# Performance work log

Measured on AMD Instinct MI355X. Metric: run time of the kernel, lower is better.

Reference implementation:

```python
import jax, jax.numpy as jnp
import numpy as np

N0, N1, N2, N3 = 8192, 32768, 65536, 65536
CUM = (N0, N0 + N1, N0 + N1 + N2, N0 + N1 + N2 + N3)  # nodes through hop k
NTOT = CUM[3]
EH = (131072, 262144, 262144)                          # edges per hop (per edge type)
ECUM = (EH[0], EH[0] + EH[1], EH[0] + EH[1] + EH[2])
ETOT = ECUM[2]
C, H, T = 64, 256, 3
HH = H // 2
B, L = 16, 512  # N0 == B * L: equal-length note sequences per graph
LN_EPS = 1e-5


def _ln(x, w, b):
    m = x.mean(-1, keepdims=True)
    v = x.var(-1, keepdims=True)
    return (x - m) / jnp.sqrt(v + LN_EPS) * w + b


def _seg_mean(msgs, dst, n):
    s = jax.ops.segment_sum(msgs, dst, num_segments=n)
    cnt = jax.ops.segment_sum(jnp.ones(dst.shape, msgs.dtype), dst, num_segments=n)
    return s / jnp.maximum(cnt, 1.0)[:, None]


def _l2(x):
    return x / jnp.maximum(jnp.linalg.norm(x, axis=-1, keepdims=True), 1e-12)


def _gru_dir(x, wih, whh, bih, bhh, reverse):
    # x: [B, Lt, Din]; torch gate order (r, z, n)
    gi = jnp.einsum('bld,gd->blg', x, wih) + bih
    gi = jnp.moveaxis(gi, 1, 0)  # [Lt, B, 3*HH]
    h0 = jnp.zeros((x.shape[0], HH), x.dtype)

    def step(h, g):
        gh = h @ whh.T + bhh
        ir, iz, in_ = jnp.split(g, 3, -1)
        hr, hz, hn = jnp.split(gh, 3, -1)
        r = jax.nn.sigmoid(ir + hr)
        z = jax.nn.sigmoid(iz + hz)
        n = jnp.tanh(in_ + r * hn)
        hnew = (1.0 - z) * n + z * h
        return hnew, hnew

    _, ys = jax.lax.scan(step, h0, gi, reverse=reverse)
    return jnp.moveaxis(ys, 0, 1)  # [B, Lt, HH]


def _bigru(x, wih, whh, bih, bhh):
    f = _gru_dir(x, wih[0], whh[0], bih[0], bhh[0], False)
    bwd = _gru_dir(x, wih[1], whh[1], bih[1], bhh[1], True)
    return jnp.concatenate([f, bwd], -1)


def _forward(x, edge_index, batch_size, sage0_proj_w, sage0_proj_b, sage0_lw, sage0_lb,
             sage0_rw, sage_lw, sage_lb, sage_rw, ln_w, ln_b,
             gru_wih0, gru_whh0, gru_bih0, gru_bhh0,
             gru_wih1, gru_whh1, gru_bih1, gru_bhh1,
             rnn_norm_w, rnn_norm_b, mlp1_w, mlp1_b, mlp_ln_w, mlp_ln_b,
             mlp2_w, mlp2_b, cat_w, cat_b):
    # ---- hybrid GRU branch on seed notes (equal lengths -> pad == reshape) ----
    xs = x[:batch_size].reshape(B, L, C)
    h = _bigru(xs, gru_wih0, gru_whh0, gru_bih0, gru_bhh0)
    h = _bigru(h, gru_wih1, gru_whh1, gru_bih1, gru_bhh1)  # inter-layer dropout: eval mode
    h = _ln(h, rnn_norm_w, rnn_norm_b)
    h = _ln(jax.nn.relu(h @ mlp1_w + mlp1_b), mlp_ln_w, mlp_ln_b) @ mlp2_w + mlp2_b
    x_rnn = h.reshape(batch_size, H)

    # ---- GNN layer 0: SAGEConv(project=True, normalize=True), hetero mean over T types ----
    feat = x
    outs = []
    for t in range(T):
        src, dst = edge_index[t, 0], edge_index[t, 1]
        xp = jax.nn.relu(feat @ sage0_proj_w[t] + sage0_proj_b[t])
        agg = _seg_mean(xp[src], dst, NTOT)
        outs.append(_l2(agg @ sage0_lw[t] + sage0_lb[t] + feat @ sage0_rw[t]))
    feat = sum(outs) / T
    feat = _ln(jax.nn.relu(feat), ln_w[0], ln_b[0])  # dropout: eval mode (identity)

    # ---- layers 1..2 with trim_to_layer: drop last sampled hop each layer ----
    n_layer = (CUM[2], CUM[1])
    e_layer = (ECUM[1], ECUM[0])
    for i in range(2):
        n, e = n_layer[i], e_layer[i]
        feat = feat[:n]
        outs = []
        for t in range(T):
            src, dst = edge_index[t, 0, :e], edge_index[t, 1, :e]
            agg = _seg_mean(feat[src], dst, n)
            outs.append(agg @ sage_lw[i, t] + sage_lb[i, t] + feat @ sage_rw[i, t])
        feat = sum(outs) / T
        if i == 0:
            feat = _ln(jax.nn.relu(feat), ln_w[1], ln_b[1])
    x_gnn = feat[:batch_size]
    return jnp.concatenate([x_rnn, x_gnn], -1) @ cat_w + cat_b


def setup_inputs():
    key = jax.random.key(0)
    ks = iter(jax.random.split(key, 64))

    def nrm(shape, fan_in):
        return jax.random.normal(next(ks), shape, jnp.float32) / float(np.sqrt(fan_in))

    # hop-structured edges: hop k has src < CUM[k+1], dst < CUM[k]
    ei = []
    for t in range(T):
        rows, cols = [], []
        for k in range(3):
            rows.append(jax.random.randint(next(ks), (EH[k],), 0, CUM[k + 1]))
            cols.append(jax.random.randint(next(ks), (EH[k],), 0, CUM[k]))
        ei.append(jnp.stack([jnp.concatenate(rows), jnp.concatenate(cols)]))
    edge_index = jnp.stack(ei).astype(jnp.int32)

    return dict(
        x=jax.random.normal(next(ks), (NTOT, C), jnp.float32),
        edge_index=edge_index,
        batch=(jnp.arange(N0) // L).astype(jnp.int32),
        batch_size=N0,
        sage0_proj_w=nrm((T, C, C), C), sage0_proj_b=jnp.zeros((T, C), jnp.float32),
        sage0_lw=nrm((T, C, H), C), sage0_lb=jnp.zeros((T, H), jnp.float32),
        sage0_rw=nrm((T, C, H), C),
        sage_lw=nrm((2, T, H, H), H), sage_lb=jnp.zeros((2, T, H), jnp.float32),
        sage_rw=nrm((2, T, H, H), H),
        ln_w=jnp.ones((2, H), jnp.float32), ln_b=jnp.zeros((2, H), jnp.float32),
        gru_wih0=nrm((2, 3 * HH, C), C), gru_whh0=nrm((2, 3 * HH, HH), HH),
        gru_bih0=jnp.zeros((2, 3 * HH), jnp.float32), gru_bhh0=jnp.zeros((2, 3 * HH), jnp.float32),
        gru_wih1=nrm((2, 3 * HH, H), H), gru_whh1=nrm((2, 3 * HH, HH), HH),
        gru_bih1=jnp.zeros((2, 3 * HH), jnp.float32), gru_bhh1=jnp.zeros((2, 3 * HH), jnp.float32),
        rnn_norm_w=jnp.ones((H,), jnp.float32), rnn_norm_b=jnp.zeros((H,), jnp.float32),
        mlp1_w=nrm((H, H), H), mlp1_b=jnp.zeros((H,), jnp.float32),
        mlp_ln_w=jnp.ones((H,), jnp.float32), mlp_ln_b=jnp.zeros((H,), jnp.float32),
        mlp2_w=nrm((H, H), H), mlp2_b=jnp.zeros((H,), jnp.float32),
        cat_w=nrm((2 * H, H), 2 * H), cat_b=jnp.zeros((H,), jnp.float32),
    )


def reference(x, edge_index, batch, batch_size, sage0_proj_w, sage0_proj_b, sage0_lw,
              sage0_lb, sage0_rw, sage_lw, sage_lb, sage_rw, ln_w, ln_b,
              gru_wih0, gru_whh0, gru_bih0, gru_bhh0, gru_wih1, gru_whh1, gru_bih1,
              gru_bhh1, rnn_norm_w, rnn_norm_b, mlp1_w, mlp1_b, mlp_ln_w, mlp_ln_b,
              mlp2_w, mlp2_b, cat_w, cat_b):
    # batch encodes 16 equal-length (512) sequences; bincount/pad == reshape above
    return _forward(x, edge_index, batch_size, sage0_proj_w, sage0_proj_b, sage0_lw,
                    sage0_lb, sage0_rw, sage_lw, sage_lb, sage_rw, ln_w, ln_b,
                    gru_wih0, gru_whh0, gru_bih0, gru_bhh0, gru_wih1, gru_whh1,
                    gru_bih1, gru_bhh1, rnn_norm_w, rnn_norm_b, mlp1_w, mlp1_b,
                    mlp_ln_w, mlp_ln_b, mlp2_w, mlp2_b, cat_w, cat_b)
```

## Files before the change

kernel.cpp:

```cpp
#include <hip/hip_runtime.h>
#include <stdint.h>

typedef unsigned short u16;
typedef __attribute__((ext_vector_type(8))) short short8;
typedef __attribute__((ext_vector_type(4))) short short4v;
typedef __attribute__((ext_vector_type(4))) float float4v;

#define DEV static __device__ __forceinline__

DEV float bf2f(u16 u){ union { unsigned int i; float f; } c; c.i = ((unsigned int)u) << 16; return c.f; }
DEV u16 f2bf(float f){ union { float ff; unsigned int i; } c; c.ff = f;
  unsigned int x = c.i; return (u16)((x + 0x7fffu + ((x >> 16) & 1u)) >> 16); }

#define MFMA16(a,b,c) __builtin_amdgcn_mfma_f32_16x16x32_bf16((a),(b),(c),0,0,0)

#define ETOTC  655360
#define TSTRIDE 155648
#define NBINS   466944

struct SM {
  u16 As[64*72];
  u16 Bs[256*72];
  float redS[4][64];
  float redQ[4][64];
  float rowA[64], rowB[64];
};

__global__ void detect_dtype(const u16* __restrict__ xs, int* __restrict__ flag){
  __shared__ int sh[256];
  int t = threadIdx.x; int cnt = 0;
  for (int i = t; i < 4096; i += 256){
    u16 u = xs[i]; int e = (u >> 7) & 0xff;
    cnt += (u == 0 || (e >= 112 && e <= 143)) ? 1 : 0;
  }
  sh[t] = cnt; __syncthreads();
  for (int d = 128; d; d >>= 1){ if (t < d) sh[t] += sh[t+d]; __syncthreads(); }
  if (t == 0) flag[0] = (sh[0] >= 3686) ? 1 : 0;
}

DEV u16 scrub(u16 v){ int e = (v >> 7) & 0xff; return (e == 0xff) ? (u16)0 : v; }

__global__ void convert_x(const void* __restrict__ xin, const int* __restrict__ flag,
                          u16* __restrict__ out){
  int i = blockIdx.x*256 + threadIdx.x;
  u16 v[4];
  if (flag[0] == 1){
    short4v s = ((const short4v*)xin)[i];
#pragma unroll
    for (int j=0;j<4;j++) v[j] = scrub((u16)s[j]);
  } else {
    float4v f = ((const float4v*)xin)[i];
#pragma unroll
    for (int j=0;j<4;j++) v[j] = scrub(f2bf(f[j]));
  }
  short4v o; o[0]=(short)v[0]; o[1]=(short)v[1]; o[2]=(short)v[2]; o[3]=(short)v[3];
  ((short4v*)out)[i] = o;
}

struct WSrc { const void* p[28]; };
__device__ const int g_wcum[29] = {0,12288,12480,61632,62400,111552,504768,506304,899520,
  900032,900544,949696,1048000,1048768,1049536,1246144,1344448,1345216,1345984,1346240,
  1346496,1412032,1412288,1412544,1412800,1478336,1478592,1609664,1609920};

__global__ void convert_w(WSrc d, const int* __restrict__ flag, u16* __restrict__ out){
  int i = blockIdx.x*256 + threadIdx.x;
  if (i >= 1609920) return;
  int lo = 0, hi = 28;
  while (hi - lo > 1){ int m = (lo+hi) >> 1; if (i >= g_wcum[m]) lo = m; else hi = m; }
  int off = i - g_wcum[lo];
  u16 v = (flag[0] == 1) ? ((const u16*)d.p[lo])[off]
                         : f2bf(((const float*)d.p[lo])[off]);
  out[i] = scrub(v);
}

__global__ void packT(const u16* __restrict__ in, u16* __restrict__ out, int K, int N){
  int i = blockIdx.x*256 + threadIdx.x;
  if (i < K*N){ int n = i / K, k = i - n*K; out[i] = in[(size_t)k*N + n]; }
}

__global__ void pack_lr(const u16* __restrict__ lw, const u16* __restrict__ rw,
                        u16* __restrict__ out, int F){
  int K2 = 2*F; long total = 3L*256*K2;
  long i = (long)blockIdx.x*256 + threadIdx.x;
  if (i < total){
    int k = (int)(i % K2); int n = (int)((i / K2) & 255); int t = (int)(i / ((long)K2*256));
    out[i] = (k < F) ? lw[((size_t)t*F + k)*256 + n]
                     : rw[((size_t)t*F + (k-F))*256 + n];
  }
}

DEV void hist_body(int gb, const int* __restrict__ ei, int* __restrict__ cnt){
  int g = gb*256 + threadIdx.x;
  int t = g / ETOTC, e = g - t*ETOTC;
  int dst = ei[(size_t)t*2*ETOTC + ETOTC + e];
  int base = t*TSTRIDE;
  atomicAdd(&cnt[base + dst], 1);
  if (e < 393216) atomicAdd(&cnt[base + 106496 + dst], 1);
  if (e < 131072) atomicAdd(&cnt[base + 147456 + dst], 1);
}

DEV void perm_body(int gb, const int* __restrict__ ei, const int* __restrict__ off,
                   int* __restrict__ slot, int* __restrict__ srcs){
  int g = gb*256 + threadIdx.x;
  int t = g / ETOTC, e = g - t*ETOTC;
  int dst = ei[(size_t)t*2*ETOTC + ETOTC + e];
  int src = ei[(size_t)t*2*ETOTC + e];
  int base = t*TSTRIDE;
  { int b = base + dst; srcs[off[b] + atomicAdd(&slot[b], 1)] = src; }
  if (e < 393216){ int b = base + 106496 + dst;
    srcs[off[b] + atomicAdd(&slot[b], 1)] = src; }
  if (e < 131072){ int b = base + 147456 + dst;
    srcs[off[b] + atomicAdd(&slot[b], 1)] = src; }
}

__global__ void scan_blocks(const int* __restrict__ cnt, int* __restrict__ off,
                            int* __restrict__ bsum, int n){
  __shared__ int sh[256];
  int t = threadIdx.x;
  int base = blockIdx.x*2048 + t*8;
  int v[8]; int tot = 0;
#pragma unroll
  for (int j=0;j<8;j++){ v[j] = (base+j < n) ? cnt[base+j] : 0; tot += v[j]; }
  sh[t] = tot; __syncthreads();
  for (int d=1; d<256; d<<=1){
    int y = (t>=d) ? sh[t-d] : 0; __syncthreads();
    sh[t] += y; __syncthreads();
  }
  int run = sh[t] - tot;
#pragma unroll
  for (int j=0;j<8;j++){ if (base+j < n) off[base+j] = run; run += v[j]; }
  if (t == 255) bsum[blockIdx.x] = sh[255];
}

__global__ void scan_top(int* __restrict__ bsum, int G){
  __shared__ int sh[256];
  int t = threadIdx.x;
  int v = (t < G) ? bsum[t] : 0;
  sh[t] = v; __syncthreads();
  for (int d=1; d<256; d<<=1){
    int y = (t>=d) ? sh[t-d] : 0; __syncthreads();
    sh[t] += y; __syncthreads();
  }
  if (t < G) bsum[t] = sh[t] - v;
}

__global__ void scan_add(int* __restrict__ off, const int* __restrict__ bsum, int n){
  int add = bsum[blockIdx.x];
  int base = blockIdx.x*2048 + threadIdx.x*8;
#pragma unroll
  for (int j=0;j<8;j++) if (base+j < n) off[base+j] += add;
}

template<int F>
DEV void gather_body(int w, int lane,
    const int* __restrict__ off, const int* __restrict__ cnt, const int* __restrict__ srcs,
    const u16* __restrict__ feat, int ld, u16* __restrict__ out)
{
  int st = off[w], c = cnt[w];
  float sc = 1.f / (float)(c < 1 ? 1 : c);
  if (F == 64) {
    float a = 0.f, b = 0.f;
    int i = 0;
    for (; i + 4 <= c; i += 4){
      int s0 = srcs[st+i], s1 = srcs[st+i+1], s2 = srcs[st+i+2], s3 = srcs[st+i+3];
      u16 u0 = feat[(size_t)s0*ld + lane];
      u16 u1 = feat[(size_t)s1*ld + lane];
      u16 u2 = feat[(size_t)s2*ld + lane];
      u16 u3 = feat[(size_t)s3*ld + lane];
      a += bf2f(u0) + bf2f(u1);
      b += bf2f(u2) + bf2f(u3);
    }
    for (; i < c; ++i){ int s = srcs[st+i]; a += bf2f(feat[(size_t)s*ld + lane]); }
    out[(size_t)w*64 + lane] = f2bf((a + b)*sc);
  } else {
    float a0=0.f,a1=0.f,a2=0.f,a3=0.f;
    float b0=0.f,b1=0.f,b2=0.f,b3=0.f;
    int i = 0;
    for (; i + 4 <= c; i += 4){
      int s0 = srcs[st+i], s1 = srcs[st+i+1], s2 = srcs[st+i+2], s3 = srcs[st+i+3];
      short4v u0 = *(const short4v*)(feat + (size_t)s0*ld + lane*4);
      short4v u1 = *(const short4v*)(feat + (size_t)s1*ld + lane*4);
      short4v u2 = *(const short4v*)(feat + (size_t)s2*ld + lane*4);
      short4v u3 = *(const short4v*)(feat + (size_t)s3*ld + lane*4);
      a0 += bf2f((u16)u0[0]) + bf2f((u16)u1[0]);
      a1 += bf2f((u16)u0[1]) + bf2f((u16)u1[1]);
      a2 += bf2f((u16)u0[2]) + bf2f((u16)u1[2]);
      a3 += bf2f((u16)u0[3]) + bf2f((u16)u1[3]);
      b0 += bf2f((u16)u2[0]) + bf2f((u16)u3[0]);
      b1 += bf2f((u16)u2[1]) + bf2f((u16)u3[1]);
      b2 += bf2f((u16)u2[2]) + bf2f((u16)u3[2]);
      b3 += bf2f((u16)u2[3]) + bf2f((u16)u3[3]);
    }
    for (; i < c; ++i){
      int s = srcs[st+i];
      short4v u = *(const short4v*)(feat + (size_t)s*ld + lane*4);
      a0 += bf2f((u16)u[0]); a1 += bf2f((u16)u[1]);
      a2 += bf2f((u16)u[2]); a3 += bf2f((u16)u[3]);
    }
    u16* o = out + (size_t)w*256 + lane*4;
    o[0]=f2bf((a0+b0)*sc); o[1]=f2bf((a1+b1)*sc);
    o[2]=f2bf((a2+b2)*sc); o[3]=f2bf((a3+b3)*sc);
  }
}

DEV void ln_body(int r, int lane,
    const u16* __restrict__ in, u16* __restrict__ out,
    const u16* __restrict__ w, const u16* __restrict__ b)
{
  short4v u = *(const short4v*)(in + (size_t)r*256 + lane*4);
  float v[4];
#pragma unroll
  for (int i=0;i<4;i++) v[i] = bf2f((u16)u[i]);
  float s = v[0]+v[1]+v[2]+v[3];
  float q = v[0]*v[0]+v[1]*v[1]+v[2]*v[2]+v[3]*v[3];
#pragma unroll
  for (int d=1; d<64; d<<=1){ s += __shfl_xor(s, d); q += __shfl_xor(q, d); }
  float mu = s * (1.f/256.f);
  float var = fmaxf(q * (1.f/256.f) - mu*mu, 0.f);
  float rs = rsqrtf(var + 1e-5f);
  u16* o = out + (size_t)r*256 + lane*4;
#pragma unroll
  for (int i=0;i<4;i++){
    int col = lane*4 + i;
    o[i] = f2bf((v[i]-mu)*rs*bf2f(w[col]) + bf2f(b[col]));
  }
}

#define LGKM0_SB do{ asm volatile("s_waitcnt lgkmcnt(0)" ::: "memory"); \
                     __builtin_amdgcn_sched_barrier(0); \
                     __builtin_amdgcn_s_barrier(); \
                     __builtin_amdgcn_sched_barrier(0); }while(0)

#define GRU_STEP(S, C0, C1, C2) do{                                          \
    const int l_ = dir ? (511 - (S)) : (S);                                  \
    short8 afr_[4];                                                          \
    _Pragma("unroll")                                                        \
    for (int kt=0; kt<4; kt++) afr_[kt] = *(const short8*)(&hbf[kt*32 + lg*8]); \
    float4v acc_[4];                                                         \
    _Pragma("unroll")                                                        \
    for (int nt=0; nt<4; nt++) acc_[nt] = (float4v){0.f,0.f,0.f,0.f};        \
    _Pragma("unroll")                                                        \
    for (int kt=0; kt<4; kt++){                                              \
      _Pragma("unroll")                                                      \
      for (int nt=0; nt<4; nt++) acc_[nt] = MFMA16(afr_[kt], bfrag[nt][kt], acc_[nt]); } \
    if (lane < 16){                                                          \
      _Pragma("unroll")                                                      \
      for (int nt=0; nt<4; nt++) ghs[64*w + nt*16 + lane] = acc_[nt][0];     \
    }                                                                        \
    LGKM0_SB;                                                                \
    if (tid < 128){                                                          \
      float ghr = ghs[tid]       + bhr;                                      \
      float ghz = ghs[128 + tid] + bhz;                                      \
      float ghn = ghs[256 + tid] + bhn;                                      \
      float r_ = 1.f/(1.f + __expf(-((C0) + ghr)));                          \
      float z_ = 1.f/(1.f + __expf(-((C1) + ghz)));                          \
      float xn_ = (C2) + r_*ghn;                                             \
      float th_ = 1.f - 2.f/(__expf(2.f*xn_) + 1.f);                         \
      hreg = (1.f - z_)*th_ + z_*hreg;                                       \
      u16 hb_ = f2bf(hreg);                                                  \
      hbf[tid] = hb_;                                                        \
      hout[((size_t)(b*512 + l_))*256 + dir*128 + tid] = hb_;                \
      int sn_ = (S) + 2;                                                     \
      if (sn_ < 512){                                                        \
        int ln2_ = dir ? (511 - sn_) : sn_;                                  \
        const float* g_ = gbase + (size_t)ln2_*768;                          \
        (C0) = g_[0]; (C1) = g_[128]; (C2) = g_[256];                        \
      }                                                                      \
    }                                                                        \
    LGKM0_SB;                                                                \
  }while(0)

DEV void gru_body(const float* __restrict__ gi, const u16* __restrict__ whh,
                  const u16* __restrict__ bhh, u16* __restrict__ hout,
                  int bid, u16* hbf, float* ghs)
{
  const int b = bid >> 1, dir = bid & 1;
  const int tid = threadIdx.x;
  const int w = tid >> 6, lane = tid & 63;
  const int lr = lane & 15, lg = lane >> 4;

  short8 bfrag[4][4];
#pragma unroll
  for (int nt=0; nt<4; nt++)
#pragma unroll
    for (int kt=0; kt<4; kt++){
      int n = 64*w + nt*16 + lr;
      bfrag[nt][kt] = *(const short8*)(whh + ((size_t)(dir*384 + n))*128 + kt*32 + lg*8);
    }

  const float* gbase = gi + (size_t)b*512*768 + dir*384 + tid;
  float hreg = 0.f, bhr = 0.f, bhz = 0.f, bhn = 0.f;
  float a0=0.f,a1=0.f,a2=0.f, e0=0.f,e1=0.f,e2=0.f;
  if (tid < 128){
    bhr = bf2f(bhh[dir*384 + tid]);
    bhz = bf2f(bhh[dir*384 + 128 + tid]);
    bhn = bf2f(bhh[dir*384 + 256 + tid]);
    const float* g0 = gbase + (size_t)(dir ? 511 : 0)*768;
    a0 = g0[0]; a1 = g0[128]; a2 = g0[256];
    const float* g1 = gbase + (size_t)(dir ? 510 : 1)*768;
    e0 = g1[0]; e1 = g1[128]; e2 = g1[256];
  }
  if (tid < 64) ((unsigned int*)hbf)[tid] = 0u;
  LGKM0_SB;

  for (int s2 = 0; s2 < 512; s2 += 2){
    GRU_STEP(s2,     a0, a1, a2);
    GRU_STEP(s2 + 1, e0, e1, e2);
  }
}

template<int F>
__global__ __launch_bounds__(384,1) void fused_gru_gather(
    const float* __restrict__ gi, const u16* __restrict__ whh,
    const u16* __restrict__ bhh, u16* __restrict__ hout,
    const int* __restrict__ off0, const int* __restrict__ cnt0, const int* __restrict__ srcs,
    const u16* __restrict__ feat, int ld, int featstep,
    u16* __restrict__ aggout, long aggstride, int rows, int bpt)
{
  __shared__ u16 hbf[128];
  __shared__ float ghs[384];
  if (blockIdx.x < 32){
    gru_body(gi, whh, bhh, hout, blockIdx.x, hbf, ghs);
    return;
  }
  int gb = blockIdx.x - 32;
  int t = gb / bpt, rb = gb - t*bpt;
  int w = rb*6 + (threadIdx.x >> 6);
  int lane = threadIdx.x & 63;
  if (w >= rows) return;
  gather_body<F>(w, lane, off0 + t*TSTRIDE, cnt0 + t*TSTRIDE, srcs,
                 feat + (size_t)t*featstep, ld, aggout + (size_t)t*aggstride);
}

template<int EPI, bool OUTF32>
DEV void gemm_body(SM& sm, int bx, int by,
    const u16* __restrict__ A, int lda,
    const u16* __restrict__ WT, int K, int N,
    const u16* __restrict__ bias,
    const u16* __restrict__ lnw, const u16* __restrict__ lnb,
    void* __restrict__ Cp, int ldc, const int* __restrict__ dynof)
{
  u16* As = sm.As; u16* Bs = sm.Bs;
  const int tid = threadIdx.x;
  const int lane = tid & 63, wid = tid >> 6;
  const int lr = lane & 15, lg = lane >> 4;
  const int m0 = bx * 64;
  const int col0 = by * 256;
  float4v acc[4][4];
#pragma unroll
  for (int i=0;i<4;i++)
#pragma unroll
    for (int j=0;j<4;j++) acc[i][j] = (float4v){0.f,0.f,0.f,0.f};

  for (int k0 = 0; k0 < K; k0 += 64){
#pragma unroll
    for (int v = 0; v < 2; v++){
      int idx = tid + v*256; int r = idx >> 3, c8 = (idx & 7) << 3;
      *(short8*)(&As[r*72 + c8]) = *(const short8*)(A + (size_t)(m0+r)*lda + k0 + c8);
    }
#pragma unroll
    for (int v = 0; v < 8; v++){
      int idx = tid + v*256; int nn = idx >> 3, c8 = (idx & 7) << 3;
      short8 val = {0,0,0,0,0,0,0,0};
      if (col0 + nn < N) val = *(const short8*)(WT + (size_t)(col0+nn)*K + k0 + c8);
      *(short8*)(&Bs[nn*72 + c8]) = val;
    }
    __syncthreads();
#pragma unroll
    for (int kk = 0; kk < 2; kk++){
      short8 af[4], bfr[4];
#pragma unroll
      for (int i=0;i<4;i++) af[i]  = *(const short8*)(&As[(16*i+lr)*72 + kk*32 + lg*8]);
#pragma unroll
      for (int j=0;j<4;j++) bfr[j] = *(const short8*)(&Bs[(wid*64+16*j+lr)*72 + kk*32 + lg*8]);
#pragma unroll
      for (int i=0;i<4;i++)
#pragma unroll
        for (int j=0;j<4;j++) acc[i][j] = MFMA16(af[i], bfr[j], acc[i][j]);
    }
    __syncthreads();
  }
  int cols[4];
#pragma unroll
  for (int j=0;j<4;j++) cols[j] = col0 + wid*64 + 16*j + lr;
#pragma unroll
  for (int j=0;j<4;j++){
    float bv = (cols[j] < N) ? bf2f(bias[cols[j]]) : 0.f;
#pragma unroll
    for (int i=0;i<4;i++)
#pragma unroll
      for (int r=0;r<4;r++) acc[i][j][r] += bv;
  }
  if (EPI >= 1){
#pragma unroll
    for (int i=0;i<4;i++)
#pragma unroll
      for (int j=0;j<4;j++)
#pragma unroll
        for (int r=0;r<4;r++) acc[i][j][r] = fmaxf(acc[i][j][r], 0.f);
  }
  if (EPI == 2){
#pragma unroll
    for (int i=0;i<4;i++)
#pragma unroll
      for (int r=0;r<4;r++){
        float p = acc[i][0][r]+acc[i][1][r]+acc[i][2][r]+acc[i][3][r];
        float q = acc[i][0][r]*acc[i][0][r]+acc[i][1][r]*acc[i][1][r]
                 +acc[i][2][r]*acc[i][2][r]+acc[i][3][r]*acc[i][3][r];
#pragma unroll
        for (int d=1; d<16; d<<=1){ p += __shfl_xor(p,d); q += __shfl_xor(q,d); }
        if (lr == 0){ sm.redS[wid][16*i + lg*4 + r] = p; sm.redQ[wid][16*i + lg*4 + r] = q; }
      }
    __syncthreads();
    if (tid < 64){
      float s = sm.redS[0][tid]+sm.redS[1][tid]+sm.redS[2][tid]+sm.redS[3][tid];
      float q = sm.redQ[0][tid]+sm.redQ[1][tid]+sm.redQ[2][tid]+sm.redQ[3][tid];
      float mu = s * (1.f/256.f);
      float var = fmaxf(q * (1.f/256.f) - mu*mu, 0.f);
      sm.rowA[tid] = mu; sm.rowB[tid] = rsqrtf(var + 1e-5f);
    }
    __syncthreads();
#pragma unroll
    for (int i=0;i<4;i++)
#pragma unroll
      for (int r=0;r<4;r++){
        int rl = 16*i + lg*4 + r;
        float mu = sm.rowA[rl], rs = sm.rowB[rl];
#pragma unroll
        for (int j=0;j<4;j++){
          float w = bf2f(lnw[cols[j]]), bb = bf2f(lnb[cols[j]]);
          acc[i][j][r] = (acc[i][j][r]-mu)*rs*w + bb;
        }
      }
  }
  bool of32 = OUTF32;
  if (dynof) of32 = (dynof[0] == 0);
#pragma unroll
  for (int i=0;i<4;i++)
#pragma unroll
    for (int r=0;r<4;r++){
      int row = m0 + 16*i + lg*4 + r;
#pragma unroll
      for (int j=0;j<4;j++) if (cols[j] < N){
        if (of32) ((float*)Cp)[(size_t)row*ldc + cols[j]] = acc[i][j][r];
        else ((u16*)Cp)[(size_t)row*ldc + cols[j]] = f2bf(acc[i][j][r]);
      }
    }
}

template<int EPI, bool OUTF32>
__global__ __launch_bounds__(256,1) void gemm_bt(
    const u16* __restrict__ A, int lda,
    const u16* __restrict__ WT, int K, int N,
    const u16* __restrict__ bias,
    const u16* __restrict__ lnw, const u16* __restrict__ lnb,
    void* __restrict__ Cp, int ldc, const int* __restrict__ dynof)
{
  __shared__ SM sm;
  gemm_body<EPI,OUTF32>(sm, blockIdx.x, blockIdx.y, A, lda, WT, K, N, bias, lnw, lnb, Cp, ldc, dynof);
}

template<int F, bool DO_L2, bool DO_LN>
DEV void sage_body(SM& sm, int bx,
    const u16* __restrict__ A1, long a1t, const u16* __restrict__ A2, int lda2,
    const u16* __restrict__ WTp, const u16* __restrict__ lbp,
    const u16* __restrict__ lnw, const u16* __restrict__ lnb,
    u16* __restrict__ out, int ldc, int outcol)
{
  constexpr int K2 = 2*F;
  u16* As = sm.As; u16* Bs = sm.Bs;
  const int tid = threadIdx.x;
  const int lane = tid & 63, wid = tid >> 6;
  const int lr = lane & 15, lg = lane >> 4;
  const int m0 = bx * 64;
  int colsL[4];
#pragma unroll
  for (int j=0;j<4;j++) colsL[j] = wid*64 + 16*j + lr;
  float4v facc[4][4];
#pragma unroll
  for (int i=0;i<4;i++)
#pragma unroll
    for (int j=0;j<4;j++) facc[i][j] = (float4v){0.f,0.f,0.f,0.f};

  for (int t=0; t<3; ++t){
    float4v acc[4][4];
#pragma unroll
    for (int i=0;i<4;i++)
#pragma unroll
      for (int j=0;j<4;j++) acc[i][j] = (float4v){0.f,0.f,0.f,0.f};
    const u16* WT  = WTp + (size_t)t*256*K2;
    const u16* A1b = A1 + (size_t)t*a1t;
    for (int k0 = 0; k0 < K2; k0 += 64){
      const u16* Ab; int la, kb;
      if (k0 < F){ Ab = A1b; la = F; kb = k0; } else { Ab = A2; la = lda2; kb = k0 - F; }
#pragma unroll
      for (int v=0; v<2; v++){
        int idx = tid + v*256; int r = idx >> 3, c8 = (idx & 7) << 3;
        *(short8*)(&As[r*72 + c8]) = *(const short8*)(Ab + (size_t)(m0+r)*la + kb + c8);
      }
#pragma unroll
      for (int v=0; v<8; v++){
        int idx = tid + v*256; int nn = idx >> 3, c8 = (idx & 7) << 3;
        *(short8*)(&Bs[nn*72 + c8]) = *(const short8*)(WT + (size_t)nn*K2 + k0 + c8);
      }
      __syncthreads();
#pragma unroll
      for (int kk = 0; kk < 2; kk++){
        short8 af[4], bfr[4];
#pragma unroll
        for (int i=0;i<4;i++) af[i]  = *(const short8*)(&As[(16*i+lr)*72 + kk*32 + lg*8]);
#pragma unroll
        for (int j=0;j<4;j++) bfr[j] = *(const short8*)(&Bs[(wid*64+16*j+lr)*72 + kk*32 + lg*8]);
#pragma unroll
        for (int i=0;i<4;i++)
#pragma unroll
          for (int j=0;j<4;j++) acc[i][j] = MFMA16(af[i], bfr[j], acc[i][j]);
      }
      __syncthreads();
    }
#pragma unroll
    for (int j=0;j<4;j++){
      float bv = bf2f(lbp[t*256 + colsL[j]]);
#pragma unroll
      for (int i=0;i<4;i++)
#pragma unroll
        for (int r=0;r<4;r++) acc[i][j][r] += bv;
    }
    if (DO_L2){
#pragma unroll
      for (int i=0;i<4;i++)
#pragma unroll
        for (int r=0;r<4;r++){
          float q = acc[i][0][r]*acc[i][0][r]+acc[i][1][r]*acc[i][1][r]
                   +acc[i][2][r]*acc[i][2][r]+acc[i][3][r]*acc[i][3][r];
#pragma unroll
          for (int d=1; d<16; d<<=1) q += __shfl_xor(q,d);
          if (lr == 0) sm.redQ[wid][16*i + lg*4 + r] = q;
        }
      __syncthreads();
      if (tid < 64){
        float q = sm.redQ[0][tid]+sm.redQ[1][tid]+sm.redQ[2][tid]+sm.redQ[3][tid];
        sm.rowA[tid] = 1.f / fmaxf(sqrtf(q), 1e-12f);
      }
      __syncthreads();
#pragma unroll
      for (int i=0;i<4;i++)
#pragma unroll
        for (int r=0;r<4;r++){
          float sc = sm.rowA[16*i + lg*4 + r];
#pragma unroll
          for (int j=0;j<4;j++) acc[i][j][r] *= sc;
        }
      __syncthreads();
    }
#pragma unroll
    for (int i=0;i<4;i++)
#pragma unroll
      for (int j=0;j<4;j++)
#pragma unroll
        for (int r=0;r<4;r++) facc[i][j][r] += acc[i][j][r];
  }
  const float inv3 = (1.f/3.f);
#pragma unroll
  for (int i=0;i<4;i++)
#pragma unroll
    for (int j=0;j<4;j++)
#pragma unroll
      for (int r=0;r<4;r++) facc[i][j][r] *= inv3;
  if (DO_LN){
#pragma unroll
    for (int i=0;i<4;i++)
#pragma unroll
      for (int j=0;j<4;j++)
#pragma unroll
        for (int r=0;r<4;r++) facc[i][j][r] = fmaxf(facc[i][j][r], 0.f);
#pragma unroll
    for (int i=0;i<4;i++)
#pragma unroll
      for (int r=0;r<4;r++){
        float p = facc[i][0][r]+facc[i][1][r]+facc[i][2][r]+facc[i][3][r];
        float q = facc[i][0][r]*facc[i][0][r]+facc[i][1][r]*facc[i][1][r]
                 +facc[i][2][r]*facc[i][2][r]+facc[i][3][r]*facc[i][3][r];
#pragma unroll
        for (int d=1; d<16; d<<=1){ p += __shfl_xor(p,d); q += __shfl_xor(q,d); }
        if (lr == 0){ sm.redS[wid][16*i + lg*4 + r] = p; sm.redQ[wid][16*i + lg*4 + r] = q; }
      }
    __syncthreads();
    if (tid < 64){
      float s = sm.redS[0][tid]+sm.redS[1][tid]+sm.redS[2][tid]+sm.redS[3][tid];
      float q = sm.redQ[0][tid]+sm.redQ[1][tid]+sm.redQ[2][tid]+sm.redQ[3][tid];
      float mu = s * (1.f/256.f);
      float var = fmaxf(q * (1.f/256.f) - mu*mu, 0.f);
      sm.rowA[tid] = mu; sm.rowB[tid] = rsqrtf(var + 1e-5f);
    }
    __syncthreads();
#pragma unroll
    for (int i=0;i<4;i++)
#pragma unroll
      for (int r=0;r<4;r++){
        int rl = 16*i + lg*4 + r;
        float mu = sm.rowA[rl], rs = sm.rowB[rl];
#pragma unroll
        for (int j=0;j<4;j++){
          float w = bf2f(lnw[colsL[j]]), bb = bf2f(lnb[colsL[j]]);
          facc[i][j][r] = (facc[i][j][r]-mu)*rs*w + bb;
        }
      }
  }
#pragma unroll
  for (int i=0;i<4;i++)
#pragma unroll
    for (int r=0;r<4;r++){
      int row = m0 + 16*i + lg*4 + r;
#pragma unroll
      for (int j=0;j<4;j++)
        out[(size_t)row*ldc + outcol + colsL[j]] = f2bf(facc[i][j][r]);
    }
}

__global__ __launch_bounds__(256,1) void fused_wih0_hist(
    const u16* __restrict__ x16, const u16* __restrict__ wih0b, const u16* __restrict__ bih0b,
    float* __restrict__ GI, const int* __restrict__ ei, int* __restrict__ CNT)
{
  __shared__ SM sm;
  int b = blockIdx.x;
  if (b < 384)
    gemm_body<0,true>(sm, b & 127, b >> 7, x16, 64, wih0b, 64, 768, bih0b,
                      nullptr, nullptr, GI, 768, nullptr);
  else
    hist_body(b - 384, ei, CNT);
}

__global__ __launch_bounds__(256,1) void fused_xp_perm(
    const u16* __restrict__ x16, const u16* __restrict__ WXP, const u16* __restrict__ projb,
    u16* __restrict__ XP3,
    const int* __restrict__ ei, const int* __restrict__ OFF,
    int* __restrict__ SLOT, int* __restrict__ SRCS)
{
  __shared__ SM sm;
  int b = blockIdx.x;
  if (b < 2688)
    gemm_body<1,false>(sm, b, 0, x16, 64, WXP, 64, 192, projb,
                       nullptr, nullptr, XP3, 192, nullptr);
  else
    perm_body(b - 2688, ei, OFF, SLOT, SRCS);
}

__global__ __launch_bounds__(256,1) void fused_gemm_sage0(
    const u16* __restrict__ H0, const u16* __restrict__ wih1b, const u16* __restrict__ bih1b,
    float* __restrict__ GI,
    const u16* __restrict__ AGGB0, const u16* __restrict__ x16, const u16* __restrict__ WP0,
    const u16* __restrict__ s0lb, const u16* __restrict__ lnw, const u16* __restrict__ lnb,
    u16* __restrict__ FEAT)
{
  __shared__ SM sm;
  int b = blockIdx.x;
  if (b < 384)
    gemm_body<0,true>(sm, b & 127, b >> 7, H0, 256, wih1b, 256, 768, bih1b,
                      nullptr, nullptr, GI, 768, nullptr);
  else
    sage_body<64,true,true>(sm, b - 384, AGGB0, (long)106496*64, x16, 64, WP0, s0lb,
                            lnw, lnb, FEAT, 256, 0);
}

__global__ __launch_bounds__(256,1) void fused_ln_sage1(
    const u16* __restrict__ AGGB1, const u16* __restrict__ FEAT, const u16* __restrict__ WP1,
    const u16* __restrict__ slb, const u16* __restrict__ lnw, const u16* __restrict__ lnb,
    u16* __restrict__ FEAT2,
    const u16* __restrict__ H1, u16* __restrict__ HA,
    const u16* __restrict__ rnw, const u16* __restrict__ rnb)
{
  __shared__ SM sm;
  int b = blockIdx.x;
  if (b < 640)
    sage_body<256,false,true>(sm, b, AGGB1, (long)40960*256, FEAT, 256, WP1, slb,
                              lnw, lnb, FEAT2, 256, 0);
  else {
    int r = (b - 640)*4 + (threadIdx.x >> 6);
    ln_body(r, threadIdx.x & 63, H1, HA, rnw, rnb);
  }
}

__global__ __launch_bounds__(256,1) void fused_mlp1_gather2(
    const u16* __restrict__ HA, const u16* __restrict__ M1T, const u16* __restrict__ mlp1b,
    const u16* __restrict__ mlnw, const u16* __restrict__ mlnb, u16* __restrict__ HB,
    const int* __restrict__ OFF, const int* __restrict__ CNT, const int* __restrict__ SRCS,
    const u16* __restrict__ FEAT2, u16* __restrict__ AGGB2)
{
  __shared__ SM sm;
  int b = blockIdx.x;
  if (b < 128){
    gemm_body<2,false>(sm, b, 0, HA, 256, M1T, 256, 256, mlp1b, mlnw, mlnb, HB, 256, nullptr);
  } else {
    int g = b - 128;
    int t = g / 2048, rb = g - t*2048;
    int w = rb*4 + (threadIdx.x >> 6);
    int lane = threadIdx.x & 63;
    if (w < 8192)
      gather_body<256>(w, lane, OFF + t*TSTRIDE + 147456, CNT + t*TSTRIDE + 147456, SRCS,
                       FEAT2, 256, AGGB2 + (size_t)t*8192*256);
  }
}

__global__ __launch_bounds__(256,1) void fused_mlp2_sage2(
    const u16* __restrict__ HB, const u16* __restrict__ M2T, const u16* __restrict__ mlp2b,
    u16* __restrict__ CAT,
    const u16* __restrict__ AGGB2, const u16* __restrict__ FEAT2, const u16* __restrict__ WP2,
    const u16* __restrict__ slb2)
{
  __shared__ SM sm;
  int b = blockIdx.x;
  if (b < 128)
    gemm_body<0,false>(sm, b, 0, HB, 256, M2T, 256, 256, mlp2b, nullptr, nullptr, CAT, 512, nullptr);
  else
    sage_body<256,false,false>(sm, b - 128, AGGB2, (long)8192*256, FEAT2, 256, WP2, slb2,
                               nullptr, nullptr, CAT, 512, 256);
}

extern "C" void kernel_launch(void* const* d_in, const int* in_sizes, int n_in,
                              void* d_out, int out_size, void* d_ws, size_t ws_size,
                              hipStream_t stream)
{
  (void)in_sizes; (void)n_in; (void)out_size;
  const int* ei = (const int*)d_in[1];

  char* ws = (char*)d_ws;
  size_t o = 0;
  auto alloc = [&](size_t b){ size_t p = o; o += (b + 255) & ~(size_t)255; return p; };
  char* RA   = ws + alloc(66060288);
  u16* XP3   = (u16*)RA;
  u16* AGGB1 = (u16*)RA;
  char* RR   = ws + alloc(41943040);
  float* GI  = (float*)RR;
  u16* H0    = (u16*)(RR + 25165824);
  u16* H1    = (u16*)(RR + 29360128);
  u16* HA    = (u16*)(RR + 33554432);
  u16* HB    = (u16*)(RR + 37748736);
  char* RB   = ws + alloc(40894464);
  u16* AGGB0 = (u16*)RB;
  u16* AGGB2 = (u16*)RB;
  u16* FEAT2 = (u16*)(RB + 12582912);
  u16* FEAT  = (u16*)(ws + alloc(106496ull*256*2));
  u16* CAT   = (u16*)(ws + alloc(8192ull*512*2));
  u16* AR    = (u16*)(ws + alloc(12619968ull*2));
  u16* WXP   = (u16*)(ws + alloc(192ull*64*2));
  u16* WP0   = (u16*)(ws + alloc(3ull*256*128*2));
  u16* WP1   = (u16*)(ws + alloc(3ull*256*512*2));
  u16* WP2   = (u16*)(ws + alloc(3ull*256*512*2));
  u16* M1T   = (u16*)(ws + alloc(256ull*256*2));
  u16* M2T   = (u16*)(ws + alloc(256ull*256*2));
  u16* CTT   = (u16*)(ws + alloc(256ull*512*2));
  int* CNT   = (int*)(ws + alloc((size_t)NBINS*4));
  int* OFF   = (int*)(ws + alloc((size_t)NBINS*4));
  int* SLOT  = (int*)(ws + alloc((size_t)NBINS*4));
  int* BSUM  = (int*)(ws + alloc(256ull*4));
  int* SRCS  = (int*)(ws + alloc(3538944ull*4));
  int* FLAG  = (int*)(ws + alloc(256));
  if (o > ws_size) return;

  u16* x16    = AR;
  u16* projw6 = AR + 11010048; u16* projb6 = AR + 11022336;
  u16* s0lw6  = AR + 11022528; u16* s0lb6  = AR + 11071680; u16* s0rw6 = AR + 11072448;
  u16* slw6   = AR + 11121600; u16* slb6   = AR + 11514816; u16* srw6  = AR + 11516352;
  u16* lnw6   = AR + 11909568; u16* lnb6   = AR + 11910080;
  u16* wih0b  = AR + 11910592; u16* whh0b  = AR + 11959744;
  u16* bih0b  = AR + 12058048; u16* bhh0b  = AR + 12058816;
  u16* wih1b  = AR + 12059584; u16* whh1b  = AR + 12256192;
  u16* bih1b  = AR + 12354496; u16* bhh1b  = AR + 12355264;
  u16* rnw6   = AR + 12356032; u16* rnb6   = AR + 12356288;
  u16* mlp1w6 = AR + 12356544; u16* mlp1b6 = AR + 12422080;
  u16* mlnw6  = AR + 12422336; u16* mlnb6  = AR + 12422592;
  u16* mlp2w6 = AR + 12422848; u16* mlp2b6 = AR + 12488384;
  u16* catw6  = AR + 12488640; u16* catb6  = AR + 12619712;

  detect_dtype<<<dim3(1),dim3(256),0,stream>>>((const u16*)d_in[0], FLAG);
  convert_x<<<dim3(10752),dim3(256),0,stream>>>(d_in[0], FLAG, x16);
  WSrc wsrc;
  for (int i=0;i<28;i++) wsrc.p[i] = d_in[4+i];
  convert_w<<<dim3(6289),dim3(256),0,stream>>>(wsrc, FLAG, AR + 11010048);

  hipMemsetAsync(CNT, 0, (size_t)NBINS*4, stream);
  hipMemsetAsync(SLOT, 0, (size_t)NBINS*4, stream);
  packT<<<dim3(256),dim3(256),0,stream>>>(mlp1w6, M1T, 256, 256);
  packT<<<dim3(256),dim3(256),0,stream>>>(mlp2w6, M2T, 256, 256);
  packT<<<dim3(512),dim3(256),0,stream>>>(catw6,  CTT, 512, 256);
  for (int t=0;t<3;t++)
    packT<<<dim3(16),dim3(256),0,stream>>>(projw6 + (size_t)t*4096, WXP + (size_t)t*4096, 64, 64);
  pack_lr<<<dim3(384),dim3(256),0,stream>>>(s0lw6, s0rw6, WP0, 64);
  pack_lr<<<dim3(1536),dim3(256),0,stream>>>(slw6,               srw6,               WP1, 256);
  pack_lr<<<dim3(1536),dim3(256),0,stream>>>(slw6 + 3ull*256*256, srw6 + 3ull*256*256, WP2, 256);

  fused_wih0_hist<<<dim3(384 + 7680),dim3(256),0,stream>>>(
      x16, wih0b, bih0b, GI, ei, CNT);

  scan_blocks<<<dim3(228),dim3(256),0,stream>>>(CNT, OFF, BSUM, NBINS);
  scan_top<<<dim3(1),dim3(256),0,stream>>>(BSUM, 228);
  scan_add<<<dim3(228),dim3(256),0,stream>>>(OFF, BSUM, NBINS);

  fused_xp_perm<<<dim3(2688 + 7680),dim3(256),0,stream>>>(
      x16, WXP, projb6, XP3, ei, OFF, SLOT, SRCS);

  fused_gru_gather<64><<<dim3(32 + 3*17750),dim3(384),0,stream>>>(
      GI, whh0b, bhh0b, H0,
      OFF, CNT, SRCS, XP3, 192, 64, AGGB0, (long)106496*64, 106496, 17750);

  fused_gemm_sage0<<<dim3(2048),dim3(256),0,stream>>>(
      H0, wih1b, bih1b, GI,
      AGGB0, x16, WP0, s0lb6, lnw6, lnb6, FEAT);

  fused_gru_gather<256><<<dim3(32 + 3*6827),dim3(384),0,stream>>>(
      GI, whh1b, bhh1b, H1,
      OFF + 106496, CNT + 106496, SRCS, FEAT, 256, 0, AGGB1, (long)40960*256, 40960, 6827);

  fused_ln_sage1<<<dim3(2688),dim3(256),0,stream>>>(
      AGGB1, FEAT, WP1, slb6, lnw6+256, lnb6+256, FEAT2,
      H1, HA, rnw6, rnb6);

  fused_mlp1_gather2<<<dim3(6272),dim3(256),0,stream>>>(
      HA, M1T, mlp1b6, mlnw6, mlnb6, HB,
      OFF, CNT, SRCS, FEAT2, AGGB2);

  fused_mlp2_sage2<<<dim3(256),dim3(256),0,stream>>>(
      HB, M2T, mlp2b6, CAT,
      AGGB2, FEAT2, WP2, slb6 + 3*256);

  gemm_bt<0,false><<<dim3(128,1),dim3(256),0,stream>>>(CAT, 512, CTT, 512, 256, catb6,
      nullptr, nullptr, d_out, 256, FLAG);
}
```

Baseline: 1.539 ms.

## Replicate GRU gate math per wave to remove second barrier per step

Each of the six waves in a GRU block now computes the gate update redundantly for all 128 hidden units and keeps its own private copy of the hidden state in LDS. The gate-scratch buffer is double-buffered by step parity. Together these let the second block-wide barrier in each timestep become a local LDS wait. This shortens the serial recurrence's critical path, at the cost of six times more transcendental work and more input loads per step.

```diff
diff --git a/kernel.cpp b/kernel.cpp
--- a/kernel.cpp
+++ b/kernel.cpp
@@ -231,8 +231,12 @@
                      __builtin_amdgcn_s_barrier(); \
                      __builtin_amdgcn_sched_barrier(0); }while(0)
 
-#define GRU_STEP(S, C0, C1, C2) do{                                          \
+#define LGKM0_ONLY do{ asm volatile("s_waitcnt lgkmcnt(0)" ::: "memory"); \
+                       __builtin_amdgcn_sched_barrier(0); }while(0)
+
+#define GRU_STEP1(S, C0, C1, C2, C3, C4, C5) do{                             \
     const int l_ = dir ? (511 - (S)) : (S);                                  \
+    float* gp_ = ghsA + ((S) & 1)*384;                                       \
     short8 afr_[4];                                                          \
     _Pragma("unroll")                                                        \
     for (int kt=0; kt<4; kt++) afr_[kt] = *(const short8*)(&hbf[kt*32 + lg*8]); \
@@ -245,39 +249,45 @@
       for (int nt=0; nt<4; nt++) acc_[nt] = MFMA16(afr_[kt], bfrag[nt][kt], acc_[nt]); } \
     if (lane < 16){                                                          \
       _Pragma("unroll")                                                      \
-      for (int nt=0; nt<4; nt++) ghs[64*w + nt*16 + lane] = acc_[nt][0];     \
+      for (int nt=0; nt<4; nt++) gp_[64*w + nt*16 + lane] = acc_[nt][0];     \
     }                                                                        \
-    LGKM0_SB;                                                                \
-    if (tid < 128){                                                          \
-      float ghr = ghs[tid]       + bhr;                                      \
-      float ghz = ghs[128 + tid] + bhz;                                      \
-      float ghn = ghs[256 + tid] + bhn;                                      \
-      float r_ = 1.f/(1.f + __expf(-((C0) + ghr)));                          \
-      float z_ = 1.f/(1.f + __expf(-((C1) + ghz)));                          \
-      float xn_ = (C2) + r_*ghn;                                             \
-      float th_ = 1.f - 2.f/(__expf(2.f*xn_) + 1.f);                         \
-      hreg = (1.f - z_)*th_ + z_*hreg;                                       \
-      u16 hb_ = f2bf(hreg);                                                  \
-      hbf[tid] = hb_;                                                        \
-      hout[((size_t)(b*512 + l_))*256 + dir*128 + tid] = hb_;                \
+    LGKM0_SB;                                \
+    {                                                                        \
+      float r0_ = 1.f/(1.f + __expf(-((C0) + gp_[i0]       + bh0)));         \
+      float z0_ = 1.f/(1.f + __expf(-((C1) + gp_[128 + i0] + bh1)));         \
+      float xn0_ = (C2) + r0_*(gp_[256 + i0] + bh2);                         \
+      float th0_ = 1.f - 2.f/(__expf(2.f*xn0_) + 1.f);                       \
+      hreg0 = (1.f - z0_)*th0_ + z0_*hreg0;                                  \
+      float r1_ = 1.f/(1.f + __expf(-((C3) + gp_[i1]       + bh3)));         \
+      float z1_ = 1.f/(1.f + __expf(-((C4) + gp_[128 + i1] + bh4)));         \
+      float xn1_ = (C5) + r1_*(gp_[256 + i1] + bh5);                         \
+      float th1_ = 1.f - 2.f/(__expf(2.f*xn1_) + 1.f);                       \
+      hreg1 = (1.f - z1_)*th1_ + z1_*hreg1;                                  \
+      u16 hb0_ = f2bf(hreg0), hb1_ = f2bf(hreg1);                            \
+      hbf[i0] = hb0_; hbf[i1] = hb1_;                                        \
+      if (w == 0){                                                           \
+        u16* op_ = hout + ((size_t)(b*512 + l_))*256 + dir*128;              \
+        op_[i0] = hb0_; op_[i1] = hb1_;                                      \
+      }                                                                      \
       int sn_ = (S) + 2;                                                     \
       if (sn_ < 512){                                                        \
-        int ln2_ = dir ? (511 - sn_) : sn_;                                  \
-        const float* g_ = gbase + (size_t)ln2_*768;                          \
-        (C0) = g_[0]; (C1) = g_[128]; (C2) = g_[256];                        \
+        const float* g_ = gq + (size_t)(dir ? (511 - sn_) : sn_)*768;        \
+        (C0)=g_[i0]; (C1)=g_[128+i0]; (C2)=g_[256+i0];                       \
+        (C3)=g_[i1]; (C4)=g_[128+i1]; (C5)=g_[256+i1];                       \
       }                                                                      \
     }                                                                        \
-    LGKM0_SB;                                                                \
+    LGKM0_ONLY;        \
   }while(0)
 
 DEV void gru_body(const float* __restrict__ gi, const u16* __restrict__ whh,
                   const u16* __restrict__ bhh, u16* __restrict__ hout,
-                  int bid, u16* hbf, float* ghs)
+                  int bid, u16* hbfA , float* ghsA )
 {
   const int b = bid >> 1, dir = bid & 1;
   const int tid = threadIdx.x;
   const int w = tid >> 6, lane = tid & 63;
   const int lr = lane & 15, lg = lane >> 4;
+  u16* hbf = hbfA + w*128;
 
   short8 bfrag[4][4];
 #pragma unroll
@@ -288,24 +298,28 @@
       bfrag[nt][kt] = *(const short8*)(whh + ((size_t)(dir*384 + n))*128 + kt*32 + lg*8);
     }
 
-  const float* gbase = gi + (size_t)b*512*768 + dir*384 + tid;
-  float hreg = 0.f, bhr = 0.f, bhz = 0.f, bhn = 0.f;
-  float a0=0.f,a1=0.f,a2=0.f, e0=0.f,e1=0.f,e2=0.f;
-  if (tid < 128){
-    bhr = bf2f(bhh[dir*384 + tid]);
-    bhz = bf2f(bhh[dir*384 + 128 + tid]);
-    bhn = bf2f(bhh[dir*384 + 256 + tid]);
-    const float* g0 = gbase + (size_t)(dir ? 511 : 0)*768;
-    a0 = g0[0]; a1 = g0[128]; a2 = g0[256];
-    const float* g1 = gbase + (size_t)(dir ? 510 : 1)*768;
-    e0 = g1[0]; e1 = g1[128]; e2 = g1[256];
-  }
-  if (tid < 64) ((unsigned int*)hbf)[tid] = 0u;
-  LGKM0_SB;
+  const int i0 = lane, i1 = lane + 64;
+  const float* gq = gi + (size_t)b*512*768 + dir*384;
+  float hreg0 = 0.f, hreg1 = 0.f;
+  float bh0 = bf2f(bhh[dir*384 + i0]);
+  float bh1 = bf2f(bhh[dir*384 + 128 + i0]);
+  float bh2 = bf2f(bhh[dir*384 + 256 + i0]);
+  float bh3 = bf2f(bhh[dir*384 + i1]);
+  float bh4 = bf2f(bhh[dir*384 + 128 + i1]);
+  float bh5 = bf2f(bhh[dir*384 + 256 + i1]);
+  float a0,a1,a2,a3,a4,a5, e0,e1,e2,e3,e4,e5;
+  {
+    const float* g0 = gq + (size_t)(dir ? 511 : 0)*768;
+    a0=g0[i0]; a1=g0[128+i0]; a2=g0[256+i0]; a3=g0[i1]; a4=g0[128+i1]; a5=g0[256+i1];
+    const float* g1 = gq + (size_t)(dir ? 510 : 1)*768;
+    e0=g1[i0]; e1=g1[128+i0]; e2=g1[256+i0]; e3=g1[i1]; e4=g1[128+i1]; e5=g1[256+i1];
+  }
+  hbf[i0] = 0; hbf[i1] = 0;
+  LGKM0_ONLY;
 
   for (int s2 = 0; s2 < 512; s2 += 2){
-    GRU_STEP(s2,     a0, a1, a2);
-    GRU_STEP(s2 + 1, e0, e1, e2);
+    GRU_STEP1(s2,     a0, a1, a2, a3, a4, a5);
+    GRU_STEP1(s2 + 1, e0, e1, e2, e3, e4, e5);
   }
 }
 
@@ -317,10 +331,10 @@
     const u16* __restrict__ feat, int ld, int featstep,
     u16* __restrict__ aggout, long aggstride, int rows, int bpt)
 {
-  __shared__ u16 hbf[128];
-  __shared__ float ghs[384];
+  __shared__ u16 hbfA[6*128];
+  __shared__ float ghsA[2*384];
   if (blockIdx.x < 32){
-    gru_body(gi, whh, bhh, hout, blockIdx.x, hbf, ghs);
+    gru_body(gi, whh, bhh, hout, blockIdx.x, hbfA, ghsA);
     return;
   }
   int gb = blockIdx.x - 32;
```

Measured after the change: 1.744 ms. 1.13x slower.
